# Kernel optimization log

Measured on AMD Instinct MI355X. Metric: run time of the kernel, lower is better.

## Reference

```python
import jax, jax.numpy as jnp
import numpy as np

B, T, D, H = 2, 2048, 1024, 16
DH = D // H


def setup_inputs() -> dict:
    key = jax.random.key(0)
    ks = jax.random.split(key, 8)
    s = 1.0 / np.sqrt(D)  # xavier-ish scale
    return {
        "query": jax.random.normal(ks[0], (B, T, D), jnp.float32),
        "key": jax.random.normal(ks[1], (B, T, D), jnp.float32),
        "value": jax.random.normal(ks[2], (B, T, D), jnp.float32),
        "Wq": jax.random.normal(ks[3], (D, D), jnp.float32) * s,
        "bq": jnp.zeros((D,), jnp.float32),
        "Wk": jax.random.normal(ks[4], (D, D), jnp.float32) * s,
        "bk": jnp.zeros((D,), jnp.float32),
        "Wv": jax.random.normal(ks[5], (D, D), jnp.float32) * s,
        "bv": jnp.zeros((D,), jnp.float32),
        "Wo": jax.random.normal(ks[6], (D, D), jnp.float32) * s,
        "bo": jnp.zeros((D,), jnp.float32),
        # causal mask (B, T, T); True = attend
        "mask": jnp.broadcast_to(jnp.tril(jnp.ones((T, T), bool)), (B, T, T)),
    }


def _split_heads(x):  # (B, T, D) -> (B, H, T, Dh)
    return x.reshape(B, T, H, DH).transpose(0, 2, 1, 3)


def reference(query, key, value, Wq, bq, Wk, bk, Wv, bv, Wo, bo, mask):
    q = _split_heads(query @ Wq + bq)
    k = _split_heads(key @ Wk + bk)
    v = _split_heads(value @ Wv + bv)
    scores = jnp.einsum("bhqd,bhkd->bhqk", q, k) / jnp.sqrt(jnp.float32(DH))
    scores = jnp.where(mask[:, None, :, :], scores, -jnp.inf)
    w = jax.nn.softmax(scores, axis=-1)
    out = jnp.einsum("bhqk,bhkd->bhqd", w, v)
    out = out.transpose(0, 2, 1, 3).reshape(B, T, D)  # merge heads
    return out @ Wo + bo
```

## Files before the change

### kernel.cpp

```cpp
#include <hip/hip_runtime.h>

typedef unsigned short u16;
typedef __attribute__((ext_vector_type(4))) float f32x4;
typedef __attribute__((ext_vector_type(8))) short bf16x8;

#define MFMA16(a,b,c) __builtin_amdgcn_mfma_f32_16x16x32_bf16((a),(b),(c),0,0,0)

__device__ inline u16 f2bf(float f){
  union { float f; unsigned u; } v; v.f = f;
  unsigned r = v.u + 0x7FFFu + ((v.u >> 16) & 1u);
  return (u16)(r >> 16);
}
__device__ inline u16 f2bf_fast(float f){
  union { float f; unsigned u; } v; v.f = f;
  return (u16)((v.u + 0x8000u) >> 16);
}
__device__ inline unsigned pk2bf(float x, float y){
  union { float f; unsigned u; } a, b; a.f=x; b.f=y;
  return ((a.u + 0x8000u)>>16) | ((b.u + 0x8000u) & 0xFFFF0000u);
}

typedef const __attribute__((address_space(1))) unsigned int* gas_ptr;
typedef __attribute__((address_space(3))) unsigned int* las_ptr;
__device__ inline void gload_lds16(const u16* g, u16* l){
  __builtin_amdgcn_global_load_lds((gas_ptr)(const void*)g, (las_ptr)(void*)l, 16, 0, 0);
}

struct PrepArgs { const float* x[3]; u16* y[3]; const float* W[4]; u16* Wt[4]; };
__global__ void k_prep(PrepArgs a){
  __shared__ u16 t[32][33];
  int blk = blockIdx.x;
  int tid = threadIdx.x;
  if (blk < 12288){
    int tn = blk >> 12;
    int i  = (blk & 4095)*256 + tid;
    float4 v = ((const float4*)a.x[tn])[i];
    ushort4 o;
    o.x = f2bf(v.x); o.y = f2bf(v.y); o.z = f2bf(v.z); o.w = f2bf(v.w);
    ((ushort4*)a.y[tn])[i] = o;
  } else {
    int w = blk - 12288;
    int z = w >> 10;
    int xy = w & 1023;
    int kb = (xy & 31)*32, nb = (xy >> 5)*32;
    const float* W = a.W[z];
    u16* Wt = a.Wt[z];
    int tx = tid & 31, ty = tid >> 5;
    #pragma unroll
    for (int i=0;i<32;i+=8)
      t[ty+i][tx] = f2bf(W[(size_t)(kb+ty+i)*1024 + nb+tx]);
    __syncthreads();
    #pragma unroll
    for (int i=0;i<32;i+=8)
      Wt[(size_t)(nb+ty+i)*1024 + kb+tx] = t[tx][ty+i];
  }
}

__global__ void k_tv(const u16* __restrict__ V, u16* __restrict__ VT){
  __shared__ u16 t[32][33];
  int tb = blockIdx.x*32;
  int db = blockIdx.y*32;
  int bh = blockIdx.z;
  int b = bh>>4, h = bh&15;
  int tx = threadIdx.x, ty = threadIdx.y;
  #pragma unroll
  for (int i=0;i<32;i+=8)
    t[ty+i][tx] = V[(size_t)(b*2048 + tb+ty+i)*1024 + h*64 + db+tx];
  __syncthreads();
  #pragma unroll
  for (int i=0;i<32;i+=8)
    VT[(size_t)(bh*64 + db+ty+i)*2048 + tb+tx] = t[tx][ty+i];
}

struct GemmArgs3 { const u16* A[3]; const u16* Bt[3]; const float* bias[3]; u16* C[3]; };

#define STAGE_A(slot, kh) { \
  int c0_ = tid, c1_ = tid + 512; \
  gload_lds16(A + (size_t)(row0 + (c0_>>2))*1024 + (kh)*32 + (((c0_&3) ^ ((c0_>>3)&3))*8), &As[slot][c0_*8]); \
  gload_lds16(A + (size_t)(row0 + (c1_>>2))*1024 + (kh)*32 + (((c1_&3) ^ ((c1_>>3)&3))*8), &As[slot][c1_*8]); }
#define STAGE_B(slot, kh) { \
  int c0_ = tid, c1_ = tid + 512; \
  gload_lds16(Bt + (size_t)(col0 + (c0_>>2))*1024 + (kh)*32 + (((c0_&3) ^ ((c0_>>3)&3))*8), &Bs[slot][c0_*8]); \
  gload_lds16(Bt + (size_t)(col0 + (c1_>>2))*1024 + (kh)*32 + (((c1_&3) ^ ((c1_>>3)&3))*8), &Bs[slot][c1_*8]); }

#define PHASE1(s, STAGE_STMT) { \
  const u16* Al = &As[s][0]; const u16* Bl = &Bs[s][0]; \
  _Pragma("unroll") \
  for (int nf=0;nf<4;nf++) \
    bfr[nf] = *(const bf16x8*)(Bl + (wc*64+nf*16+lo)*32 + pg*8); \
  _Pragma("unroll") \
  for (int mf=0;mf<4;mf++) \
    af[mf] = *(const bf16x8*)(Al + (wr*128+mf*16+lo)*32 + pg*8); \
  STAGE_STMT \
  __builtin_amdgcn_s_barrier(); \
  asm volatile("s_waitcnt lgkmcnt(0)" ::: "memory"); \
  __builtin_amdgcn_s_setprio(1); \
  _Pragma("unroll") \
  for (int mf=0;mf<4;mf++) \
    _Pragma("unroll") \
    for (int nf=0;nf<4;nf++) \
      acc[mf][nf] = MFMA16(af[mf], bfr[nf], acc[mf][nf]); \
  __builtin_amdgcn_s_setprio(0); \
  __builtin_amdgcn_s_barrier(); }

#define PHASE2(s, STAGE_STMT, VM_STMT) { \
  const u16* Al = &As[s][0]; \
  _Pragma("unroll") \
  for (int mf=0;mf<4;mf++) \
    af[mf] = *(const bf16x8*)(Al + (wr*128+(mf+4)*16+lo)*32 + pg*8); \
  STAGE_STMT \
  VM_STMT \
  __builtin_amdgcn_s_barrier(); \
  asm volatile("s_waitcnt lgkmcnt(0)" ::: "memory"); \
  __builtin_amdgcn_s_setprio(1); \
  _Pragma("unroll") \
  for (int mf=0;mf<4;mf++) \
    _Pragma("unroll") \
    for (int nf=0;nf<4;nf++) \
      acc[mf+4][nf] = MFMA16(af[mf], bfr[nf], acc[mf+4][nf]); \
  __builtin_amdgcn_s_setprio(0); \
  __builtin_amdgcn_s_barrier(); }

__global__ __launch_bounds__(512) void k_gemm3(GemmArgs3 g){
  const int N=1024;
  __shared__ __attribute__((aligned(16))) u16 As[4][256*32];
  __shared__ __attribute__((aligned(16))) u16 Bs[4][256*32];
  int flat = blockIdx.x;
  int swz = (flat&7)*24 + (flat>>3);
  int bz = swz>>6, rem = swz&63;
  int bx = rem>>2, by = rem&3;
  const u16* A = g.A[bz]; const u16* Bt = g.Bt[bz];
  const float* bias = g.bias[bz]; u16* C = g.C[bz];
  const int tid = threadIdx.x;
  const int wave = tid>>6, lane = tid&63;
  const int lo = lane&15, hi = lane>>4;
  const int wr = wave>>2, wc = wave&3;
  const int row0 = bx*256, col0 = by*256;
  const int pg = hi ^ ((lo>>1)&3);

  f32x4 acc[8][4];
  #pragma unroll
  for (int i=0;i<8;i++)
    #pragma unroll
    for (int j=0;j<4;j++) acc[i][j] = (f32x4){0.f,0.f,0.f,0.f};

  STAGE_A(0,0); STAGE_B(0,0);
  STAGE_A(1,1); STAGE_B(1,1);
  STAGE_A(2,2); STAGE_B(2,2);
  asm volatile("s_waitcnt vmcnt(8)" ::: "memory");
  __builtin_amdgcn_s_barrier();

  bf16x8 bfr[4], af[4];
  for (int h = 0; h < 29; ++h){
    const int s = h & 3;
    const int s3 = (h+3) & 3;
    PHASE1(s, STAGE_A(s3, h+3);)
    PHASE2(s, STAGE_B(s3, h+3);, asm volatile("s_waitcnt vmcnt(8)" ::: "memory");)
  }
  PHASE1(1, )
  PHASE2(1, , asm volatile("s_waitcnt vmcnt(4)" ::: "memory");)
  PHASE1(2, )
  PHASE2(2, , asm volatile("s_waitcnt vmcnt(0)" ::: "memory");)
  PHASE1(3, )
  PHASE2(3, , )

  #pragma unroll
  for (int mf=0;mf<8;mf++){
    #pragma unroll
    for (int nf=0;nf<4;nf++){
      int r0 = row0 + wr*128 + mf*16 + hi*4;
      int c0 = col0 + wc*64 + nf*16 + lo;
      float bv = bias[c0];
      #pragma unroll
      for (int r=0;r<4;r++)
        C[(size_t)(r0+r)*N + c0] = f2bf(acc[mf][nf][r] + bv);
    }
  }
}

__global__ __launch_bounds__(256) void k_gemmO(const u16* __restrict__ A, const u16* __restrict__ Bt,
                                               const float* __restrict__ bias, float* __restrict__ C){
  const int N=1024, K=1024;
  int f = blockIdx.x;
  int xcd = f & 7, idx = f >> 3;
  int bx = xcd*8 + (idx>>3), by = idx & 7;
  __shared__ __attribute__((aligned(16))) u16 As[64*64];
  __shared__ __attribute__((aligned(16))) u16 Bs[128*64];
  const int tid  = threadIdx.x;
  const int wave = tid>>6, lane = tid&63;
  const int lo = lane&15, hi = lane>>4;
  const int row0 = bx*64, col0 = by*128;
  const int wm = (wave>>1)*32, wn = (wave&1)*64;
  f32x4 acc[2][4];
  #pragma unroll
  for (int i=0;i<2;i++)
    #pragma unroll
    for (int j=0;j<4;j++) acc[i][j] = (f32x4){0.f,0.f,0.f,0.f};

  for (int k0=0; k0<K; k0+=64){
    #pragma unroll
    for (int r=0;r<2;r++){
      int c = r*256 + tid;
      gload_lds16(A + (size_t)(row0 + (c>>3))*K + k0 + (c&7)*8, As + c*8);
    }
    #pragma unroll
    for (int r=0;r<4;r++){
      int c = r*256 + tid;
      gload_lds16(Bt + (size_t)(col0 + (c>>3))*K + k0 + (c&7)*8, Bs + c*8);
    }
    __syncthreads();
    __builtin_amdgcn_s_setprio(1);
    #pragma unroll
    for (int ks=0;ks<2;ks++){
      bf16x8 af[2], bfr[4];
      #pragma unroll
      for (int mf=0;mf<2;mf++)
        af[mf] = *(const bf16x8*)(As + (wm+mf*16+lo)*64 + ks*32 + hi*8);
      #pragma unroll
      for (int nf=0;nf<4;nf++)
        bfr[nf] = *(const bf16x8*)(Bs + (wn+nf*16+lo)*64 + ks*32 + hi*8);
      #pragma unroll
      for (int mf=0;mf<2;mf++)
        #pragma unroll
        for (int nf=0;nf<4;nf++)
          acc[mf][nf] = MFMA16(af[mf], bfr[nf], acc[mf][nf]);
    }
    __builtin_amdgcn_s_setprio(0);
    __syncthreads();
  }
  #pragma unroll
  for (int mf=0;mf<2;mf++){
    #pragma unroll
    for (int nf=0;nf<4;nf++){
      int r0 = row0 + wm + mf*16 + hi*4;
      int c0 = col0 + wn + nf*16 + lo;
      float bv = bias[c0];
      #pragma unroll
      for (int r=0;r<4;r++)
        C[(size_t)(r0+r)*N + c0] = acc[mf][nf][r] + bv;
    }
  }
}

__global__ __launch_bounds__(256) void k_attn(
    const u16* __restrict__ Q, const u16* __restrict__ Kp,
    const u16* __restrict__ VT, u16* __restrict__ O)
{
  const int T=2048, D=1024;
  __shared__ __attribute__((aligned(16))) u16 Ks[2][64*64];
  __shared__ __attribute__((aligned(16))) u16 Vs[2][64*64];
  __shared__ __attribute__((aligned(16))) u16 Plds[4][16*64];
  int f = blockIdx.x + (blockIdx.y<<5);
  int xcd = f & 7, idx = f >> 3;
  const int bh = (xcd<<2) | (idx&3);
  const int qb = 31 - (idx>>2);
  const int b = bh>>4, h = bh&15;
  const int tid = threadIdx.x;
  const int wave = tid>>6, lane = tid&63;
  const int lo = lane&15, hi = lane>>4;
  const int wi = wave>>1, wj = wave&1;
  const int lo7 = lo&7;
  const float NEG = -1e30f;
  const float sc = 0.125f * 1.44269504f;
  const float MC = 64.0f * sc;
  const bf16x8 ones = {0x3F80,0x3F80,0x3F80,0x3F80,0x3F80,0x3F80,0x3F80,0x3F80};

  const int c0 = tid, c1 = 256 + tid;
  const int sr0 = c0>>3, sj0 = (c0&7)^(sr0&7);
  const int sr1 = c1>>3, sj1 = (c1&7)^(sr1&7);
  const u16* Kbase = Kp + (size_t)(b*T)*D + h*64;
  const u16* Vbase = VT + (size_t)(bh*64)*T;
  const size_t kOff0 = (size_t)sr0*D + sj0*8, kOff1 = (size_t)sr1*D + sj1*8;
  const size_t vOff0 = (size_t)sr0*T + sj0*8, vOff1 = (size_t)sr1*T + sj1*8;

  const int qrow0 = qb*64 + wi*32;
  bf16x8 qf[2][2];
  #pragma unroll
  for (int qnf=0;qnf<2;qnf++){
    const u16* Qr = Q + (size_t)(b*T + qrow0 + qnf*16 + lo)*D + h*64;
    qf[qnf][0] = *(const bf16x8*)(Qr + hi*8);
    qf[qnf][1] = *(const bf16x8*)(Qr + 32 + hi*8);
  }

  f32x4 o[2][4];
  #pragma unroll
  for (int i=0;i<2;i++)
    #pragma unroll
    for (int j=0;j<4;j++) o[i][j] = (f32x4){0.f,0.f,0.f,0.f};
  f32x4 lac[2];
  lac[0] = (f32x4){0.f,0.f,0.f,0.f};
  lac[1] = (f32x4){0.f,0.f,0.f,0.f};

  gload_lds16(Kbase + kOff0, &Ks[0][c0*8]);
  gload_lds16(Kbase + kOff1, &Ks[0][c1*8]);
  gload_lds16(Vbase + vOff0, &Vs[0][c0*8]);
  gload_lds16(Vbase + vOff1, &Vs[0][c1*8]);
  __syncthreads();

  u16* Pl = &Plds[wave][0];
  const int kcof0 = ((     hi) ^ lo7)*8;
  const int kcof1 = (( 4 + hi) ^ lo7)*8;
  const int vcof  = ((wj*4+hi) ^ lo7)*8;

  int cur = 0;
  for (int kb=0; kb<=qb; kb++){
    if (kb < qb){
      const u16* Kt = Kbase + (size_t)(kb+1)*64*D;
      const u16* Vt = Vbase + (kb+1)*64;
      gload_lds16(Kt + kOff0, &Ks[cur^1][c0*8]);
      gload_lds16(Kt + kOff1, &Ks[cur^1][c1*8]);
      gload_lds16(Vt + vOff0, &Vs[cur^1][c0*8]);
      gload_lds16(Vt + vOff1, &Vs[cur^1][c1*8]);
    }
    const u16* Kl = Ks[cur];
    const u16* Vl = Vs[cur];
    f32x4 s[2][2];
    __builtin_amdgcn_s_setprio(1);
    #pragma unroll
    for (int knf=0;knf<2;knf++){
      int krow = wj*32 + knf*16 + lo;
      bf16x8 kf0 = *(const bf16x8*)(Kl + krow*64 + kcof0);
      bf16x8 kf1 = *(const bf16x8*)(Kl + krow*64 + kcof1);
      #pragma unroll
      for (int qnf=0;qnf<2;qnf++){
        f32x4 z = (f32x4){0.f,0.f,0.f,0.f};
        z = MFMA16(kf0, qf[qnf][0], z);
        s[knf][qnf] = MFMA16(kf1, qf[qnf][1], z);
      }
    }
    __builtin_amdgcn_s_setprio(0);
    if (kb == qb){
      int ql = wi*32 + lo;
      #pragma unroll
      for (int knf=0;knf<2;knf++){
        int kl0 = wj*32 + knf*16 + 4*hi;
        #pragma unroll
        for (int qnf=0;qnf<2;qnf++){
          int qv = ql + qnf*16;
          #pragma unroll
          for (int r=0;r<4;r++)
            if (kl0 + r > qv) s[knf][qnf][r] = NEG;
        }
      }
    }
    #pragma unroll
    for (int knf=0;knf<2;knf++)
      #pragma unroll
      for (int qnf=0;qnf<2;qnf++){
        float p0 = __builtin_amdgcn_exp2f(__builtin_fmaf(s[knf][qnf][0], sc, -MC));
        float p1 = __builtin_amdgcn_exp2f(__builtin_fmaf(s[knf][qnf][1], sc, -MC));
        float p2 = __builtin_amdgcn_exp2f(__builtin_fmaf(s[knf][qnf][2], sc, -MC));
        float p3 = __builtin_amdgcn_exp2f(__builtin_fmaf(s[knf][qnf][3], sc, -MC));
        unsigned w0 = pk2bf(p0, p1);
        unsigned w1 = pk2bf(p2, p3);
        int gphys = (qnf*4 + knf*2 + (hi>>1)) ^ lo7;
        uint2 wv; wv.x = w0; wv.y = w1;
        *(uint2*)&Pl[lo*64 + gphys*8 + 4*(hi&1)] = wv;
      }
    bf16x8 pa0 = *(const bf16x8*)&Pl[lo*64 + kcof0];
    bf16x8 pa1 = *(const bf16x8*)&Pl[lo*64 + kcof1];
    __builtin_amdgcn_s_setprio(1);
    lac[0] = MFMA16(pa0, ones, lac[0]);
    lac[1] = MFMA16(pa1, ones, lac[1]);
    #pragma unroll
    for (int dhnf=0;dhnf<4;dhnf++){
      bf16x8 vf = *(const bf16x8*)(Vl + (dhnf*16+lo)*64 + vcof);
      o[0][dhnf] = MFMA16(pa0, vf, o[0][dhnf]);
      o[1][dhnf] = MFMA16(pa1, vf, o[1][dhnf]);
    }
    __builtin_amdgcn_s_setprio(0);
    __syncthreads();
    cur ^= 1;
  }
  float* os  = (float*)&Ks[0][0];
  float* lsc = (float*)&Vs[0][0];
  if (wj == 1){
    #pragma unroll
    for (int qnf=0;qnf<2;qnf++){
      #pragma unroll
      for (int dhnf=0;dhnf<4;dhnf++)
        #pragma unroll
        for (int r=0;r<4;r++)
          os[((wi*32 + qnf*16 + 4*hi + r)<<6) + dhnf*16 + lo] = o[qnf][dhnf][r];
      if (lo == 0)
        #pragma unroll
        for (int r=0;r<4;r++)
          lsc[wi*32 + qnf*16 + 4*hi + r] = lac[qnf][r];
    }
  }
  __syncthreads();
  if (wj == 0){
    #pragma unroll
    for (int qnf=0;qnf<2;qnf++)
      #pragma unroll
      for (int r=0;r<4;r++){
        int qloc = wi*32 + qnf*16 + 4*hi + r;
        float lt = lac[qnf][r] + lsc[qloc];
        float rinv = 1.0f / lt;
        #pragma unroll
        for (int dhnf=0;dhnf<4;dhnf++){
          float val = o[qnf][dhnf][r] + os[(qloc<<6) + dhnf*16 + lo];
          O[(size_t)(b*T + qb*64 + qloc)*D + h*64 + dhnf*16 + lo] = f2bf_fast(val * rinv);
        }
      }
  }
}

extern "C" void kernel_launch(void* const* d_in, const int* in_sizes, int n_in,
                              void* d_out, int out_size, void* d_ws, size_t ws_size,
                              hipStream_t stream) {
  const int B=2, T=2048, D=1024;
  const int M = B*T;
  const float* query = (const float*)d_in[0];
  const float* key   = (const float*)d_in[1];
  const float* value = (const float*)d_in[2];
  const float* Wq = (const float*)d_in[3];  const float* bq = (const float*)d_in[4];
  const float* Wk = (const float*)d_in[5];  const float* bk = (const float*)d_in[6];
  const float* Wv = (const float*)d_in[7];  const float* bv = (const float*)d_in[8];
  const float* Wo = (const float*)d_in[9];  const float* bo = (const float*)d_in[10];
  float* out = (float*)d_out;

  char* ws = (char*)d_ws;
  const size_t MB = 1024*1024;
  u16* xq  = (u16*)(ws + 0*MB);
  u16* xk  = (u16*)(ws + 8*MB);
  u16* xv  = (u16*)(ws + 16*MB);
  u16* WqT = (u16*)(ws + 24*MB);
  u16* WkT = (u16*)(ws + 26*MB);
  u16* WvT = (u16*)(ws + 28*MB);
  u16* WoT = (u16*)(ws + 30*MB);
  u16* Qp  = (u16*)(ws + 32*MB);
  u16* Kp  = (u16*)(ws + 40*MB);
  u16* Vp  = (u16*)(ws + 48*MB);
  u16* VTp = (u16*)(ws + 56*MB);
  u16* AO  = (u16*)(ws + 64*MB);

  PrepArgs pa;
  pa.x[0]=query; pa.x[1]=key; pa.x[2]=value;
  pa.y[0]=xq; pa.y[1]=xk; pa.y[2]=xv;
  pa.W[0]=Wq; pa.W[1]=Wk; pa.W[2]=Wv; pa.W[3]=Wo;
  pa.Wt[0]=WqT; pa.Wt[1]=WkT; pa.Wt[2]=WvT; pa.Wt[3]=WoT;
  k_prep<<<16384, 256, 0, stream>>>(pa);

  GemmArgs3 ga;
  ga.A[0]=xq; ga.A[1]=xk; ga.A[2]=xv;
  ga.Bt[0]=WqT; ga.Bt[1]=WkT; ga.Bt[2]=WvT;
  ga.bias[0]=bq; ga.bias[1]=bk; ga.bias[2]=bv;
  ga.C[0]=Qp; ga.C[1]=Kp; ga.C[2]=Vp;
  k_gemm3<<<192, 512, 0, stream>>>(ga);

  k_tv<<<dim3(T/32, 2, 32), dim3(32,8), 0, stream>>>(Vp, VTp);
  k_attn<<<dim3(32,32), 256, 0, stream>>>(Qp, Kp, VTp, AO);
  k_gemmO<<<512, 256, 0, stream>>>(AO, WoT, bo, out);
}
```

Before: 113.3 us.

## Software-pipeline QK^T one tile ahead of softmax and PV in attention loop

```diff
diff --git a/kernel.cpp b/kernel.cpp
--- a/kernel.cpp
+++ b/kernel.cpp
@@ -291,30 +291,25 @@
   lac[0] = (f32x4){0.f,0.f,0.f,0.f};
   lac[1] = (f32x4){0.f,0.f,0.f,0.f};
 
+  u16* Pl = &Plds[wave][0];
+  const int kcof0 = ((     hi) ^ lo7)*8;
+  const int kcof1 = (( 4 + hi) ^ lo7)*8;
+  const int vcof  = ((wj*4+hi) ^ lo7)*8;
+
   gload_lds16(Kbase + kOff0, &Ks[0][c0*8]);
   gload_lds16(Kbase + kOff1, &Ks[0][c1*8]);
   gload_lds16(Vbase + vOff0, &Vs[0][c0*8]);
   gload_lds16(Vbase + vOff1, &Vs[0][c1*8]);
+  {
+    const u16* Kt = Kbase + (size_t)64*D;
+    gload_lds16(Kt + kOff0, &Ks[1][c0*8]);
+    gload_lds16(Kt + kOff1, &Ks[1][c1*8]);
+  }
   __syncthreads();
 
-  u16* Pl = &Plds[wave][0];
-  const int kcof0 = ((     hi) ^ lo7)*8;
-  const int kcof1 = (( 4 + hi) ^ lo7)*8;
-  const int vcof  = ((wj*4+hi) ^ lo7)*8;
-
-  int cur = 0;
-  for (int kb=0; kb<=qb; kb++){
-    if (kb < qb){
-      const u16* Kt = Kbase + (size_t)(kb+1)*64*D;
-      const u16* Vt = Vbase + (kb+1)*64;
-      gload_lds16(Kt + kOff0, &Ks[cur^1][c0*8]);
-      gload_lds16(Kt + kOff1, &Ks[cur^1][c1*8]);
-      gload_lds16(Vt + vOff0, &Vs[cur^1][c0*8]);
-      gload_lds16(Vt + vOff1, &Vs[cur^1][c1*8]);
-    }
-    const u16* Kl = Ks[cur];
-    const u16* Vl = Vs[cur];
-    f32x4 s[2][2];
+  f32x4 scur[2][2], snext[2][2];
+  {
+    const u16* Kl = Ks[0];
     __builtin_amdgcn_s_setprio(1);
     #pragma unroll
     for (int knf=0;knf<2;knf++){
@@ -325,10 +320,41 @@
       for (int qnf=0;qnf<2;qnf++){
         f32x4 z = (f32x4){0.f,0.f,0.f,0.f};
         z = MFMA16(kf0, qf[qnf][0], z);
-        s[knf][qnf] = MFMA16(kf1, qf[qnf][1], z);
+        scur[knf][qnf] = MFMA16(kf1, qf[qnf][1], z);
       }
     }
     __builtin_amdgcn_s_setprio(0);
+  }
+  __syncthreads();
+
+  for (int kb=0; kb<=qb; kb++){
+    if (kb+1 <= qb){
+      const u16* Vt = Vbase + (kb+1)*64;
+      gload_lds16(Vt + vOff0, &Vs[(kb+1)&1][c0*8]);
+      gload_lds16(Vt + vOff1, &Vs[(kb+1)&1][c1*8]);
+    }
+    if (kb+2 <= qb){
+      const u16* Kt = Kbase + (size_t)(kb+2)*64*D;
+      gload_lds16(Kt + kOff0, &Ks[kb&1][c0*8]);
+      gload_lds16(Kt + kOff1, &Ks[kb&1][c1*8]);
+    }
+    if (kb+1 <= qb){
+      const u16* Kl = Ks[(kb+1)&1];
+      __builtin_amdgcn_s_setprio(1);
+      #pragma unroll
+      for (int knf=0;knf<2;knf++){
+        int krow = wj*32 + knf*16 + lo;
+        bf16x8 kf0 = *(const bf16x8*)(Kl + krow*64 + kcof0);
+        bf16x8 kf1 = *(const bf16x8*)(Kl + krow*64 + kcof1);
+        #pragma unroll
+        for (int qnf=0;qnf<2;qnf++){
+          f32x4 z = (f32x4){0.f,0.f,0.f,0.f};
+          z = MFMA16(kf0, qf[qnf][0], z);
+          snext[knf][qnf] = MFMA16(kf1, qf[qnf][1], z);
+        }
+      }
+      __builtin_amdgcn_s_setprio(0);
+    }
     if (kb == qb){
       int ql = wi*32 + lo;
       #pragma unroll
@@ -339,7 +365,7 @@
           int qv = ql + qnf*16;
           #pragma unroll
           for (int r=0;r<4;r++)
-            if (kl0 + r > qv) s[knf][qnf][r] = NEG;
+            if (kl0 + r > qv) scur[knf][qnf][r] = NEG;
         }
       }
     }
@@ -347,10 +373,10 @@
     for (int knf=0;knf<2;knf++)
       #pragma unroll
       for (int qnf=0;qnf<2;qnf++){
-        float p0 = __builtin_amdgcn_exp2f(__builtin_fmaf(s[knf][qnf][0], sc, -MC));
-        float p1 = __builtin_amdgcn_exp2f(__builtin_fmaf(s[knf][qnf][1], sc, -MC));
-        float p2 = __builtin_amdgcn_exp2f(__builtin_fmaf(s[knf][qnf][2], sc, -MC));
-        float p3 = __builtin_amdgcn_exp2f(__builtin_fmaf(s[knf][qnf][3], sc, -MC));
+        float p0 = __builtin_amdgcn_exp2f(__builtin_fmaf(scur[knf][qnf][0], sc, -MC));
+        float p1 = __builtin_amdgcn_exp2f(__builtin_fmaf(scur[knf][qnf][1], sc, -MC));
+        float p2 = __builtin_amdgcn_exp2f(__builtin_fmaf(scur[knf][qnf][2], sc, -MC));
+        float p3 = __builtin_amdgcn_exp2f(__builtin_fmaf(scur[knf][qnf][3], sc, -MC));
         unsigned w0 = pk2bf(p0, p1);
         unsigned w1 = pk2bf(p2, p3);
         int gphys = (qnf*4 + knf*2 + (hi>>1)) ^ lo7;
@@ -359,6 +385,7 @@
       }
     bf16x8 pa0 = *(const bf16x8*)&Pl[lo*64 + kcof0];
     bf16x8 pa1 = *(const bf16x8*)&Pl[lo*64 + kcof1];
+    const u16* Vl = Vs[kb&1];
     __builtin_amdgcn_s_setprio(1);
     lac[0] = MFMA16(pa0, ones, lac[0]);
     lac[1] = MFMA16(pa1, ones, lac[1]);
@@ -370,7 +397,11 @@
     }
     __builtin_amdgcn_s_setprio(0);
     __syncthreads();
-    cur ^= 1;
+    #pragma unroll
+    for (int knf=0;knf<2;knf++)
+      #pragma unroll
+      for (int qnf=0;qnf<2;qnf++)
+        scur[knf][qnf] = snext[knf][qnf];
   }
   float* os  = (float*)&Ks[0][0];
   float* lsc = (float*)&Vs[0][0];
```

Result: no change. 114.7 us (+1.2%).
